# Kernel optimization log

Measured on AMD Instinct MI355X. Metric: run time of the kernel, lower is better.

The kernel has to match this reference:

```python
import jax, jax.numpy as jnp
import numpy as np

NUM_REGIONS = 196
NHEAD = 8
EPS = 1e-8  # torch F.cosine_similarity eps


def _mha(q_in, k_in, v_in, w_in, w_out):
    # q_in,k_in,v_in: (L,B,d); w_in: (3d,d); w_out: (d,d); bias=False, eval (no dropout)
    L, B, d = q_in.shape
    hd = d // NHEAD
    wq, wk, wv = w_in[:d], w_in[d:2 * d], w_in[2 * d:]

    def split_heads(x, w):
        y = x @ w.T  # (L,B,d)
        return jnp.transpose(y.reshape(x.shape[0], B, NHEAD, hd), (1, 2, 0, 3))  # (B,H,L,hd)

    q = split_heads(q_in, wq) * (1.0 / np.sqrt(hd)).astype(q_in.dtype)
    k = split_heads(k_in, wk)
    v = split_heads(v_in, wv)
    attn = jax.nn.softmax(jnp.einsum('bhqd,bhkd->bhqk', q, k), axis=-1)
    out = jnp.einsum('bhqk,bhkd->bhqd', attn, v)  # (B,H,L,hd)
    out = jnp.transpose(out, (2, 0, 1, 3)).reshape(L, B, d)
    return out @ w_out.T


def _window_agg(text, window, anchor):
    # text: (B,T,C); window size W=window (odd); anchor: (B,T,C)
    B, T, C = text.shape
    pad = window // 2
    padded = jnp.pad(text, ((0, 0), (pad, pad), (0, 0)))
    # (B,T,W,C): window k-th element for output pos j is padded[:, j+k]
    win = jnp.stack([padded[:, k:k + T] for k in range(window)], axis=2)
    dot = jnp.einsum('btc,btwc->btw', anchor, win)
    na = jnp.linalg.norm(anchor, axis=-1)          # (B,T)
    nw = jnp.linalg.norm(win, axis=-1)             # (B,T,W)
    weight = dot / (jnp.maximum(na, EPS)[..., None] * jnp.maximum(nw, EPS))
    return jnp.einsum('btw,btwc->btc', weight, win)


def setup_inputs() -> dict:
    key = jax.random.key(0)
    ks = jax.random.split(key, 10)
    L, B, d = 512, 32, 768
    s = 1.0 / np.sqrt(d)
    inp = {
        'query': jax.random.normal(ks[0], (L, B, d), jnp.float32),
        'key': jax.random.normal(ks[1], (L, B, d), jnp.float32),
        'value': jax.random.normal(ks[2], (L, B, d), jnp.float32),
        'w_in1': jax.random.normal(ks[3], (3 * d, d), jnp.float32) * s,
        'w_out1': jax.random.normal(ks[4], (d, d), jnp.float32) * s,
        'w_in2': jax.random.normal(ks[5], (3 * d, d), jnp.float32) * s,
        'w_out2': jax.random.normal(ks[6], (d, d), jnp.float32) * s,
        'w_in3': jax.random.normal(ks[7], (3 * d, d), jnp.float32) * s,
        'w_out3': jax.random.normal(ks[8], (d, d), jnp.float32) * s,
        'alpha': jnp.float32(1.0),
        'beta': jnp.float32(1.0),
        'gamma': jnp.float32(1.0),
    }
    return inp


def reference(query, key, value, w_in1, w_out1, w_in2, w_out2, w_in3, w_out3, alpha, beta, gamma):
    # query/key/value: (L,B,C)
    q_blc = jnp.transpose(query, (1, 0, 2))  # (B,L,C)
    visual = q_blc[:, :NUM_REGIONS]
    text = q_blc[:, NUM_REGIONS:]             # (B,T,C)

    # two-neighbor: anchor is the token itself
    two = _window_agg(text, 3, text)
    # three-neighbor: original code uses padded_two[:, i] with i=j+2, i.e. text shifted
    # left by one with a trailing zero row (faithful to the source's indexing)
    anchor3 = jnp.concatenate([text[:, 1:], jnp.zeros_like(text[:, :1])], axis=1)
    three = _window_agg(text, 5, anchor3)

    two_q = jnp.transpose(jnp.concatenate([visual, two], axis=1), (1, 0, 2))    # (L,B,C)
    three_q = jnp.transpose(jnp.concatenate([visual, three], axis=1), (1, 0, 2))

    out1 = _mha(query, key, value, w_in1, w_out1)
    out2 = _mha(two_q, key, value, w_in2, w_out2)
    out3 = _mha(three_q, key, value, w_in3, w_out3)
    return alpha * out1 + beta * out2 + gamma * out3
```

## Files before the change

### kernel.cpp

```cpp
#include <hip/hip_runtime.h>
#include <cstdint>
#include <cstddef>

typedef __bf16 bf16_t;
typedef float f32x4 __attribute__((ext_vector_type(4)));
typedef __bf16 bf16x8 __attribute__((ext_vector_type(8)));

#define MFMA_BF16(a, b, c) __builtin_amdgcn_mfma_f32_16x16x32_bf16((a), (b), (c), 0, 0, 0)

__global__ void convert_kernel(const float* __restrict__ src,
                               bf16_t* __restrict__ dst, int n8)
{
    const int i = blockIdx.x * blockDim.x + threadIdx.x;
    if (i < n8) {
        const float4* s = (const float4*)src + (size_t)i * 2;
        const float4 a = s[0], b = s[1];
        bf16x8 v = {(bf16_t)a.x, (bf16_t)a.y, (bf16_t)a.z, (bf16_t)a.w,
                    (bf16_t)b.x, (bf16_t)b.y, (bf16_t)b.z, (bf16_t)b.w};
        *((bf16x8*)dst + i) = v;
    }
}

template <typename CT>
__global__ __launch_bounds__(256) void gemm_bt(const bf16_t* __restrict__ A,
                                               const bf16_t* __restrict__ W,
                                               CT* C,
                                               int M, int N, int K,
                                               const float* __restrict__ scale_ptr,
                                               int accumulate)
{
    __shared__ bf16_t As[128 * 32];
    __shared__ bf16_t Ws[128 * 32];
    const int t = threadIdx.x;
    const int lane = t & 63;
    const int w = t >> 6;
    const int wr = (w >> 1) * 64;
    const int wc = (w & 1) * 64;
    const int tm = blockIdx.x * 128, tn = blockIdx.y * 128;
    const int l15 = lane & 15, l4 = lane >> 4;

    const f32x4 fzero = {0.f, 0.f, 0.f, 0.f};
    f32x4 acc[4][4];
    for (int i = 0; i < 4; ++i)
        for (int j = 0; j < 4; ++j) acc[i][j] = fzero;

    const int f0 = t * 8, f1 = f0 + 2048;
    const int ar0 = f0 >> 5, ac0 = f0 & 31;
    const int ar1 = f1 >> 5, ac1 = f1 & 31;

    for (int kb = 0; kb < K; kb += 32) {
        bf16x8 a0 = *(const bf16x8*)(A + (size_t)(tm + ar0) * K + kb + ac0);
        bf16x8 a1 = *(const bf16x8*)(A + (size_t)(tm + ar1) * K + kb + ac1);
        bf16x8 w0 = *(const bf16x8*)(W + (size_t)(tn + ar0) * K + kb + ac0);
        bf16x8 w1 = *(const bf16x8*)(W + (size_t)(tn + ar1) * K + kb + ac1);
        __syncthreads();
        *(bf16x8*)(As + f0) = a0;
        *(bf16x8*)(As + f1) = a1;
        *(bf16x8*)(Ws + f0) = w0;
        *(bf16x8*)(Ws + f1) = w1;
        __syncthreads();
        bf16x8 af[4], bfr[4];
#pragma unroll
        for (int i = 0; i < 4; ++i)
            af[i] = *(const bf16x8*)(As + (wr + i * 16 + l15) * 32 + l4 * 8);
#pragma unroll
        for (int j = 0; j < 4; ++j)
            bfr[j] = *(const bf16x8*)(Ws + (wc + j * 16 + l15) * 32 + l4 * 8);
#pragma unroll
        for (int i = 0; i < 4; ++i)
#pragma unroll
            for (int j = 0; j < 4; ++j)
                acc[i][j] = MFMA_BF16(af[i], bfr[j], acc[i][j]);
    }

    const float scale = scale_ptr ? scale_ptr[0] : 1.0f;
    for (int i = 0; i < 4; ++i) {
        for (int j = 0; j < 4; ++j) {
            const int col = tn + wc + j * 16 + l15;
            for (int r = 0; r < 4; ++r) {
                const int row = tm + wr + i * 16 + l4 * 4 + r;
                const size_t idx = (size_t)row * N + col;
                float v = acc[i][j][r] * scale;
                if (accumulate) v += (float)C[idx];
                C[idx] = (CT)v;
            }
        }
    }
}

__global__ __launch_bounds__(256) void attn_kernel(bf16_t* QC,
                                                   const bf16_t* __restrict__ Kp,
                                                   const bf16_t* __restrict__ Vp)
{
    constexpr int B = 32, HD = 96, D = 768;
    __shared__ bf16_t Ks[64 * 96];
    __shared__ bf16_t Vt[96 * 64];
    __shared__ bf16_t Ps[4 * 16 * 64];

    const int qt = blockIdx.x, h = blockIdx.y, b = blockIdx.z;
    const int t = threadIdx.x, lane = t & 63, w = t >> 6;
    const int l15 = lane & 15, l4 = lane >> 4;
    const int q0 = qt * 64 + w * 16;
    const float qk_scale = 0.10206207261596575f;

    bf16x8 aq[3];
#pragma unroll
    for (int kk = 0; kk < 3; ++kk)
        aq[kk] = *(const bf16x8*)(QC + ((size_t)(q0 + l15) * B + b) * D + h * HD + kk * 32 + l4 * 8);

    const f32x4 fzero = {0.f, 0.f, 0.f, 0.f};
    f32x4 o[6];
#pragma unroll
    for (int f = 0; f < 6; ++f) o[f] = fzero;
    float mr[4], lr[4];
#pragma unroll
    for (int r = 0; r < 4; ++r) { mr[r] = -1e30f; lr[r] = 0.f; }

    for (int kt = 0; kt < 8; ++kt) {
        const int k0 = kt * 64;
        bf16x8 kreg[3], vreg[3];
        int rrs[3], ccs[3];
#pragma unroll
        for (int i = 0; i < 3; ++i) {
            const int f = t * 8 + i * 2048;
            const int rr = f / 96, cc = f % 96;
            rrs[i] = rr; ccs[i] = cc;
            kreg[i] = *(const bf16x8*)(Kp + ((size_t)(k0 + rr) * B + b) * D + h * HD + cc);
            vreg[i] = *(const bf16x8*)(Vp + ((size_t)(k0 + rr) * B + b) * D + h * HD + cc);
        }
        __syncthreads();
#pragma unroll
        for (int i = 0; i < 3; ++i) {
            *(bf16x8*)(Ks + rrs[i] * 96 + ccs[i]) = kreg[i];
#pragma unroll
            for (int j = 0; j < 8; ++j)
                Vt[(ccs[i] + j) * 64 + rrs[i]] = vreg[i][j];
        }
        __syncthreads();

        f32x4 s[4];
#pragma unroll
        for (int n = 0; n < 4; ++n) {
            s[n] = fzero;
#pragma unroll
            for (int kk = 0; kk < 3; ++kk) {
                bf16x8 kf = *(const bf16x8*)(Ks + (n * 16 + l15) * 96 + kk * 32 + l4 * 8);
                s[n] = MFMA_BF16(aq[kk], kf, s[n]);
            }
        }

        float pm[4];
#pragma unroll
        for (int r = 0; r < 4; ++r) {
            float v = fmaxf(fmaxf(s[0][r], s[1][r]), fmaxf(s[2][r], s[3][r]));
            v *= qk_scale;
            v = fmaxf(v, __shfl_xor(v, 1));
            v = fmaxf(v, __shfl_xor(v, 2));
            v = fmaxf(v, __shfl_xor(v, 4));
            v = fmaxf(v, __shfl_xor(v, 8));
            pm[r] = v;
        }
        float corr[4];
        float p[4][4];
#pragma unroll
        for (int r = 0; r < 4; ++r) {
            const float mnew = fmaxf(mr[r], pm[r]);
            corr[r] = __expf(mr[r] - mnew);
            mr[r] = mnew;
            float ps = 0.f;
#pragma unroll
            for (int n = 0; n < 4; ++n) {
                const float pv = __expf(s[n][r] * qk_scale - mnew);
                p[n][r] = pv;
                ps += pv;
            }
            ps += __shfl_xor(ps, 1);
            ps += __shfl_xor(ps, 2);
            ps += __shfl_xor(ps, 4);
            ps += __shfl_xor(ps, 8);
            lr[r] = lr[r] * corr[r] + ps;
        }
#pragma unroll
        for (int f = 0; f < 6; ++f)
#pragma unroll
            for (int r = 0; r < 4; ++r) o[f][r] *= corr[r];

#pragma unroll
        for (int n = 0; n < 4; ++n)
#pragma unroll
            for (int r = 0; r < 4; ++r)
                Ps[w * 1024 + (l4 * 4 + r) * 64 + n * 16 + l15] = (bf16_t)p[n][r];
        asm volatile("s_waitcnt lgkmcnt(0)" ::: "memory");

#pragma unroll
        for (int kk = 0; kk < 2; ++kk) {
            bf16x8 pa = *(const bf16x8*)(Ps + w * 1024 + l15 * 64 + kk * 32 + l4 * 8);
#pragma unroll
            for (int f = 0; f < 6; ++f) {
                bf16x8 vb = *(const bf16x8*)(Vt + (f * 16 + l15) * 64 + kk * 32 + l4 * 8);
                o[f] = MFMA_BF16(pa, vb, o[f]);
            }
        }
    }

#pragma unroll
    for (int f = 0; f < 6; ++f)
#pragma unroll
        for (int r = 0; r < 4; ++r) {
            const int row = q0 + l4 * 4 + r;
            QC[((size_t)row * B + b) * D + h * HD + f * 16 + l15] = (bf16_t)(o[f][r] / lr[r]);
        }
}

__global__ void window_kernel(const float* __restrict__ q,
                              bf16_t* __restrict__ two_q,
                              bf16_t* __restrict__ three_q)
{
    constexpr int T = 316, B = 32, D = 768, NR = 196;
    constexpr float EPS = 1e-8f;
    const int tp = blockIdx.x, b = blockIdx.y, lane = threadIdx.x;

    float val[5][12];
#pragma unroll
    for (int w = 0; w < 5; ++w) {
        const int tt = tp + w - 2;
        const bool ok = (tt >= 0 && tt < T);
#pragma unroll
        for (int j = 0; j < 12; ++j) {
            const int c = lane + 64 * j;
            val[w][j] = ok ? q[((size_t)(NR + tt) * B + b) * D + c] : 0.f;
        }
    }
    float nrm[5], d2[3], d3[5];
#pragma unroll
    for (int w = 0; w < 5; ++w) {
        float s = 0.f;
        for (int j = 0; j < 12; ++j) s += val[w][j] * val[w][j];
        nrm[w] = s;
    }
#pragma unroll
    for (int k = 0; k < 3; ++k) {
        float s = 0.f;
        for (int j = 0; j < 12; ++j) s += val[2][j] * val[k + 1][j];
        d2[k] = s;
    }
#pragma unroll
    for (int k = 0; k < 5; ++k) {
        float s = 0.f;
        for (int j = 0; j < 12; ++j) s += val[3][j] * val[k][j];
        d3[k] = s;
    }
#pragma unroll
    for (int w = 0; w < 5; ++w)
        for (int m = 1; m < 64; m <<= 1) nrm[w] += __shfl_xor(nrm[w], m);
#pragma unroll
    for (int k = 0; k < 3; ++k)
        for (int m = 1; m < 64; m <<= 1) d2[k] += __shfl_xor(d2[k], m);
#pragma unroll
    for (int k = 0; k < 5; ++k)
        for (int m = 1; m < 64; m <<= 1) d3[k] += __shfl_xor(d3[k], m);

    const float na2 = fmaxf(sqrtf(nrm[2]), EPS);
    const float na3 = fmaxf(sqrtf(nrm[3]), EPS);
    float w2[3], w3[5];
#pragma unroll
    for (int k = 0; k < 3; ++k) w2[k] = d2[k] / (na2 * fmaxf(sqrtf(nrm[k + 1]), EPS));
#pragma unroll
    for (int k = 0; k < 5; ++k) w3[k] = d3[k] / (na3 * fmaxf(sqrtf(nrm[k]), EPS));

#pragma unroll
    for (int j = 0; j < 12; ++j) {
        float o2 = 0.f, o3 = 0.f;
#pragma unroll
        for (int k = 0; k < 3; ++k) o2 += w2[k] * val[k + 1][j];
#pragma unroll
        for (int k = 0; k < 5; ++k) o3 += w3[k] * val[k][j];
        const int c = lane + 64 * j;
        const size_t idx = ((size_t)(NR + tp) * B + b) * D + c;
        two_q[idx] = (bf16_t)o2;
        three_q[idx] = (bf16_t)o3;
    }
}

__global__ void copy_visual(const bf16_t* __restrict__ qb,
                            bf16_t* __restrict__ two_q,
                            bf16_t* __restrict__ three_q)
{
    const size_t i = (size_t)blockIdx.x * blockDim.x + threadIdx.x;
    const size_t n = (size_t)196 * 32 * 768 / 8;
    if (i < n) {
        bf16x8 v = *((const bf16x8*)qb + i);
        *((bf16x8*)two_q + i) = v;
        *((bf16x8*)three_q + i) = v;
    }
}

extern "C" void kernel_launch(void* const* d_in, const int* in_sizes, int n_in,
                              void* d_out, int out_size, void* d_ws, size_t ws_size,
                              hipStream_t stream)
{
    const float* query  = (const float*)d_in[0];
    const float* key    = (const float*)d_in[1];
    const float* value  = (const float*)d_in[2];
    const float* w_in[3]  = {(const float*)d_in[3], (const float*)d_in[5], (const float*)d_in[7]};
    const float* w_out[3] = {(const float*)d_in[4], (const float*)d_in[6], (const float*)d_in[8]};
    const float* alpha  = (const float*)d_in[9];
    const float* beta   = (const float*)d_in[10];
    const float* gamma  = (const float*)d_in[11];
    float* out = (float*)d_out;

    const size_t NE = (size_t)512 * 32 * 768;
    const size_t WSZ = (size_t)768 * 768;
    bf16_t* qb      = (bf16_t*)d_ws;
    bf16_t* kb      = qb + NE;
    bf16_t* vb      = kb + NE;
    bf16_t* two_q   = vb + NE;
    bf16_t* three_q = two_q + NE;
    bf16_t* QP      = three_q + NE;
    bf16_t* KP      = QP + NE;
    bf16_t* VP      = KP + NE;
    bf16_t* wb_in[3]  = {VP + NE, VP + NE + 3 * WSZ, VP + NE + 6 * WSZ};
    bf16_t* wb_out[3] = {VP + NE + 9 * WSZ, VP + NE + 10 * WSZ, VP + NE + 11 * WSZ};

    const int cb = 256;
    convert_kernel<<<(int)(NE / 8 + cb - 1) / cb, cb, 0, stream>>>(query, qb, (int)(NE / 8));
    convert_kernel<<<(int)(NE / 8 + cb - 1) / cb, cb, 0, stream>>>(key, kb, (int)(NE / 8));
    convert_kernel<<<(int)(NE / 8 + cb - 1) / cb, cb, 0, stream>>>(value, vb, (int)(NE / 8));
    for (int i = 0; i < 3; ++i) {
        convert_kernel<<<(int)(3 * WSZ / 8 + cb - 1) / cb, cb, 0, stream>>>(w_in[i], wb_in[i], (int)(3 * WSZ / 8));
        convert_kernel<<<(int)(WSZ / 8 + cb - 1) / cb, cb, 0, stream>>>(w_out[i], wb_out[i], (int)(WSZ / 8));
    }

    const int M = 512 * 32, D = 768;
    const dim3 ggrid(M / 128, D / 128);

    copy_visual<<<2352, 256, 0, stream>>>(qb, two_q, three_q);
    window_kernel<<<dim3(316, 32), 64, 0, stream>>>(query, two_q, three_q);

    const bf16_t* qins[3] = {two_q, three_q, qb};
    const int     wsel[3] = {1, 2, 0};
    for (int i = 0; i < 3; ++i) {
        const int s = wsel[i];
        gemm_bt<bf16_t><<<ggrid, 256, 0, stream>>>(qins[i], wb_in[s], QP, M, D, D, nullptr, 0);
        gemm_bt<bf16_t><<<ggrid, 256, 0, stream>>>(kb, wb_in[s] + WSZ, KP, M, D, D, nullptr, 0);
        gemm_bt<bf16_t><<<ggrid, 256, 0, stream>>>(vb, wb_in[s] + 2 * WSZ, VP, M, D, D, nullptr, 0);
        attn_kernel<<<dim3(8, 8, 32), 256, 0, stream>>>(QP, KP, VP);
        const float* sc = (s == 0) ? alpha : (s == 1) ? beta : gamma;
        gemm_bt<float><<<ggrid, 256, 0, stream>>>(QP, wb_out[s], out, M, D, D, sc, i > 0 ? 1 : 0);
    }
}
```

Baseline: 1.106 ms.

## Restructure attention to process full sequence per block; use direct global-to-LDS loads in GEMM

The attention kernel now gives each block one (head, batch) pair with 8 waves, and each wave handles 64 query rows as four 16-row tiles. Each K/V tile is loaded into shared memory once for all 512 queries instead of once per 64-query block, and each K/V fragment read from LDS feeds two query tiles. The V-transpose and P buffers get XOR swizzling to reduce LDS bank conflicts. The GEMM and the attention K-tile load switch to global_load_lds so data goes straight to LDS without passing through registers. In exchange, the grid shrinks from 2048 to 256 blocks and per-thread register use rises, which may limit occupancy and latency hiding.

```diff
diff --git a/kernel.cpp b/kernel.cpp
--- a/kernel.cpp
+++ b/kernel.cpp
@@ -7,6 +7,10 @@
 typedef __bf16 bf16x8 __attribute__((ext_vector_type(8)));
 
 #define MFMA_BF16(a, b, c) __builtin_amdgcn_mfma_f32_16x16x32_bf16((a), (b), (c), 0, 0, 0)
+
+#define GLDS16(gp, lp) __builtin_amdgcn_global_load_lds(                      \
+    (const __attribute__((address_space(1))) void*)(gp),                      \
+    (__attribute__((address_space(3))) void*)(lp), 16, 0, 0)
 
 __global__ void convert_kernel(const float* __restrict__ src,
                                bf16_t* __restrict__ dst, int n8)
@@ -41,23 +45,20 @@
 
     const f32x4 fzero = {0.f, 0.f, 0.f, 0.f};
     f32x4 acc[4][4];
+#pragma unroll
     for (int i = 0; i < 4; ++i)
+#pragma unroll
         for (int j = 0; j < 4; ++j) acc[i][j] = fzero;
 
-    const int f0 = t * 8, f1 = f0 + 2048;
-    const int ar0 = f0 >> 5, ac0 = f0 & 31;
-    const int ar1 = f1 >> 5, ac1 = f1 & 31;
+    const int ar0 = t >> 2, ac0 = (t & 3) * 8;
+    const int ar1 = ar0 + 64;
 
     for (int kb = 0; kb < K; kb += 32) {
-        bf16x8 a0 = *(const bf16x8*)(A + (size_t)(tm + ar0) * K + kb + ac0);
-        bf16x8 a1 = *(const bf16x8*)(A + (size_t)(tm + ar1) * K + kb + ac1);
-        bf16x8 w0 = *(const bf16x8*)(W + (size_t)(tn + ar0) * K + kb + ac0);
-        bf16x8 w1 = *(const bf16x8*)(W + (size_t)(tn + ar1) * K + kb + ac1);
         __syncthreads();
-        *(bf16x8*)(As + f0) = a0;
-        *(bf16x8*)(As + f1) = a1;
-        *(bf16x8*)(Ws + f0) = w0;
-        *(bf16x8*)(Ws + f1) = w1;
+        GLDS16(A + (size_t)(tm + ar0) * K + kb + ac0, (char*)As + w * 1024);
+        GLDS16(A + (size_t)(tm + ar1) * K + kb + ac0, (char*)As + 4096 + w * 1024);
+        GLDS16(W + (size_t)(tn + ar0) * K + kb + ac0, (char*)Ws + w * 1024);
+        GLDS16(W + (size_t)(tn + ar1) * K + kb + ac0, (char*)Ws + 4096 + w * 1024);
         __syncthreads();
         bf16x8 af[4], bfr[4];
 #pragma unroll
@@ -74,9 +75,12 @@
     }
 
     const float scale = scale_ptr ? scale_ptr[0] : 1.0f;
+#pragma unroll
     for (int i = 0; i < 4; ++i) {
+#pragma unroll
         for (int j = 0; j < 4; ++j) {
             const int col = tn + wc + j * 16 + l15;
+#pragma unroll
             for (int r = 0; r < 4; ++r) {
                 const int row = tm + wr + i * 16 + l4 * 4 + r;
                 const size_t idx = (size_t)row * N + col;
@@ -88,128 +92,151 @@
     }
 }
 
-__global__ __launch_bounds__(256) void attn_kernel(bf16_t* QC,
-                                                   const bf16_t* __restrict__ Kp,
-                                                   const bf16_t* __restrict__ Vp)
+__global__ __launch_bounds__(512, 2) void attn_kernel(bf16_t* QC,
+                                                      const bf16_t* __restrict__ Kp,
+                                                      const bf16_t* __restrict__ Vp)
 {
     constexpr int B = 32, HD = 96, D = 768;
     __shared__ bf16_t Ks[64 * 96];
     __shared__ bf16_t Vt[96 * 64];
-    __shared__ bf16_t Ps[4 * 16 * 64];
-
-    const int qt = blockIdx.x, h = blockIdx.y, b = blockIdx.z;
+    __shared__ bf16_t Ps[8][2][16 * 64];
+
+    const int h = blockIdx.x, b = blockIdx.y;
     const int t = threadIdx.x, lane = t & 63, w = t >> 6;
     const int l15 = lane & 15, l4 = lane >> 4;
-    const int q0 = qt * 64 + w * 16;
     const float qk_scale = 0.10206207261596575f;
 
-    bf16x8 aq[3];
-#pragma unroll
-    for (int kk = 0; kk < 3; ++kk)
-        aq[kk] = *(const bf16x8*)(QC + ((size_t)(q0 + l15) * B + b) * D + h * HD + kk * 32 + l4 * 8);
+    bf16x8 aq[4][3];
+#pragma unroll
+    for (int m = 0; m < 4; ++m)
+#pragma unroll
+        for (int kk = 0; kk < 3; ++kk)
+            aq[m][kk] = *(const bf16x8*)(QC + ((size_t)(w * 64 + m * 16 + l15) * B + b) * D
+                                         + h * HD + kk * 32 + l4 * 8);
 
     const f32x4 fzero = {0.f, 0.f, 0.f, 0.f};
-    f32x4 o[6];
-#pragma unroll
-    for (int f = 0; f < 6; ++f) o[f] = fzero;
-    float mr[4], lr[4];
-#pragma unroll
-    for (int r = 0; r < 4; ++r) { mr[r] = -1e30f; lr[r] = 0.f; }
+    f32x4 o[4][6];
+#pragma unroll
+    for (int m = 0; m < 4; ++m)
+#pragma unroll
+        for (int f = 0; f < 6; ++f) o[m][f] = fzero;
+    float mr[4][4], lr[4][4];
+#pragma unroll
+    for (int m = 0; m < 4; ++m)
+#pragma unroll
+        for (int r = 0; r < 4; ++r) { mr[m][r] = -1e30f; lr[m][r] = 0.f; }
+
+    const int f0 = t * 8;
+    const int rr0 = f0 / 96, cc0 = f0 % 96;
+    const int f1 = 4096 + t * 8;
+    const int rr1 = f1 / 96, cc1 = f1 % 96;
+    const int sv0 = ((cc0 >> 3) & 7) << 3;
+    const int sv1 = ((cc1 >> 3) & 7) << 3;
 
     for (int kt = 0; kt < 8; ++kt) {
         const int k0 = kt * 64;
-        bf16x8 kreg[3], vreg[3];
-        int rrs[3], ccs[3];
-#pragma unroll
-        for (int i = 0; i < 3; ++i) {
-            const int f = t * 8 + i * 2048;
-            const int rr = f / 96, cc = f % 96;
-            rrs[i] = rr; ccs[i] = cc;
-            kreg[i] = *(const bf16x8*)(Kp + ((size_t)(k0 + rr) * B + b) * D + h * HD + cc);
-            vreg[i] = *(const bf16x8*)(Vp + ((size_t)(k0 + rr) * B + b) * D + h * HD + cc);
-        }
         __syncthreads();
-#pragma unroll
-        for (int i = 0; i < 3; ++i) {
-            *(bf16x8*)(Ks + rrs[i] * 96 + ccs[i]) = kreg[i];
+        GLDS16(Kp + ((size_t)(k0 + rr0) * B + b) * D + h * HD + cc0,
+               (char*)Ks + w * 1024);
+        if (w < 4)
+            GLDS16(Kp + ((size_t)(k0 + rr1) * B + b) * D + h * HD + cc1,
+                   (char*)Ks + 8192 + w * 1024);
+        bf16x8 v0 = *(const bf16x8*)(Vp + ((size_t)(k0 + rr0) * B + b) * D + h * HD + cc0);
+        {
+            const int colsw = rr0 ^ sv0;
 #pragma unroll
             for (int j = 0; j < 8; ++j)
-                Vt[(ccs[i] + j) * 64 + rrs[i]] = vreg[i][j];
+                Vt[(cc0 + j) * 64 + colsw] = v0[j];
+        }
+        if (w < 4) {
+            bf16x8 v1 = *(const bf16x8*)(Vp + ((size_t)(k0 + rr1) * B + b) * D + h * HD + cc1);
+            const int colsw = rr1 ^ sv1;
+#pragma unroll
+            for (int j = 0; j < 8; ++j)
+                Vt[(cc1 + j) * 64 + colsw] = v1[j];
         }
         __syncthreads();
 
-        f32x4 s[4];
-#pragma unroll
-        for (int n = 0; n < 4; ++n) {
-            s[n] = fzero;
-#pragma unroll
-            for (int kk = 0; kk < 3; ++kk) {
-                bf16x8 kf = *(const bf16x8*)(Ks + (n * 16 + l15) * 96 + kk * 32 + l4 * 8);
-                s[n] = MFMA_BF16(aq[kk], kf, s[n]);
+#pragma unroll
+        for (int mp = 0; mp < 2; ++mp) {
+            f32x4 s[2][4];
+#pragma unroll
+            for (int mi = 0; mi < 2; ++mi)
+#pragma unroll
+                for (int n = 0; n < 4; ++n) s[mi][n] = fzero;
+#pragma unroll
+            for (int kk = 0; kk < 3; ++kk)
+#pragma unroll
+                for (int n = 0; n < 4; ++n) {
+                    bf16x8 kf = *(const bf16x8*)(Ks + (n * 16 + l15) * 96 + kk * 32 + l4 * 8);
+                    s[0][n] = MFMA_BF16(aq[2 * mp][kk], kf, s[0][n]);
+                    s[1][n] = MFMA_BF16(aq[2 * mp + 1][kk], kf, s[1][n]);
+                }
+#pragma unroll
+            for (int mi = 0; mi < 2; ++mi) {
+                const int m = 2 * mp + mi;
+#pragma unroll
+                for (int r = 0; r < 4; ++r) {
+                    float v = fmaxf(fmaxf(s[mi][0][r], s[mi][1][r]),
+                                    fmaxf(s[mi][2][r], s[mi][3][r]));
+                    v *= qk_scale;
+                    v = fmaxf(v, __shfl_xor(v, 1));
+                    v = fmaxf(v, __shfl_xor(v, 2));
+                    v = fmaxf(v, __shfl_xor(v, 4));
+                    v = fmaxf(v, __shfl_xor(v, 8));
+                    const float mnew = fmaxf(mr[m][r], v);
+                    const float corr = __expf(mr[m][r] - mnew);
+                    mr[m][r] = mnew;
+                    const int row = 4 * l4 + r;
+                    float ps = 0.f;
+#pragma unroll
+                    for (int n = 0; n < 4; ++n) {
+                        const float pv = __expf(s[mi][n][r] * qk_scale - mnew);
+                        ps += pv;
+                        Ps[w][mi][row * 64 + ((n * 16 + l15) ^ ((row & 7) << 3))] = (bf16_t)pv;
+                    }
+                    ps += __shfl_xor(ps, 1);
+                    ps += __shfl_xor(ps, 2);
+                    ps += __shfl_xor(ps, 4);
+                    ps += __shfl_xor(ps, 8);
+                    lr[m][r] = lr[m][r] * corr + ps;
+#pragma unroll
+                    for (int f = 0; f < 6; ++f) o[m][f][r] *= corr;
+                }
             }
-        }
-
-        float pm[4];
-#pragma unroll
-        for (int r = 0; r < 4; ++r) {
-            float v = fmaxf(fmaxf(s[0][r], s[1][r]), fmaxf(s[2][r], s[3][r]));
-            v *= qk_scale;
-            v = fmaxf(v, __shfl_xor(v, 1));
-            v = fmaxf(v, __shfl_xor(v, 2));
-            v = fmaxf(v, __shfl_xor(v, 4));
-            v = fmaxf(v, __shfl_xor(v, 8));
-            pm[r] = v;
-        }
-        float corr[4];
-        float p[4][4];
-#pragma unroll
-        for (int r = 0; r < 4; ++r) {
-            const float mnew = fmaxf(mr[r], pm[r]);
-            corr[r] = __expf(mr[r] - mnew);
-            mr[r] = mnew;
-            float ps = 0.f;
-#pragma unroll
-            for (int n = 0; n < 4; ++n) {
-                const float pv = __expf(s[n][r] * qk_scale - mnew);
-                p[n][r] = pv;
-                ps += pv;
+            asm volatile("s_waitcnt lgkmcnt(0)" ::: "memory");
+            __builtin_amdgcn_sched_barrier(0);
+            bf16x8 pa[2][2];
+#pragma unroll
+            for (int mi = 0; mi < 2; ++mi)
+#pragma unroll
+                for (int kk = 0; kk < 2; ++kk)
+                    pa[mi][kk] = *(const bf16x8*)(&Ps[w][mi][l15 * 64 +
+                                  ((kk * 32 + l4 * 8) ^ ((l15 & 7) << 3))]);
+#pragma unroll
+            for (int f = 0; f < 6; ++f) {
+                const int c = f * 16 + l15;
+                const int sv = ((c >> 3) & 7) << 3;
+#pragma unroll
+                for (int kk = 0; kk < 2; ++kk) {
+                    bf16x8 vbf = *(const bf16x8*)(Vt + c * 64 + ((kk * 32 + l4 * 8) ^ sv));
+                    o[2 * mp][f]     = MFMA_BF16(pa[0][kk], vbf, o[2 * mp][f]);
+                    o[2 * mp + 1][f] = MFMA_BF16(pa[1][kk], vbf, o[2 * mp + 1][f]);
+                }
             }
-            ps += __shfl_xor(ps, 1);
-            ps += __shfl_xor(ps, 2);
-            ps += __shfl_xor(ps, 4);
-            ps += __shfl_xor(ps, 8);
-            lr[r] = lr[r] * corr[r] + ps;
-        }
+        }
+    }
+
+#pragma unroll
+    for (int m = 0; m < 4; ++m)
 #pragma unroll
         for (int f = 0; f < 6; ++f)
 #pragma unroll
-            for (int r = 0; r < 4; ++r) o[f][r] *= corr[r];
-
-#pragma unroll
-        for (int n = 0; n < 4; ++n)
-#pragma unroll
-            for (int r = 0; r < 4; ++r)
-                Ps[w * 1024 + (l4 * 4 + r) * 64 + n * 16 + l15] = (bf16_t)p[n][r];
-        asm volatile("s_waitcnt lgkmcnt(0)" ::: "memory");
-
-#pragma unroll
-        for (int kk = 0; kk < 2; ++kk) {
-            bf16x8 pa = *(const bf16x8*)(Ps + w * 1024 + l15 * 64 + kk * 32 + l4 * 8);
-#pragma unroll
-            for (int f = 0; f < 6; ++f) {
-                bf16x8 vb = *(const bf16x8*)(Vt + (f * 16 + l15) * 64 + kk * 32 + l4 * 8);
-                o[f] = MFMA_BF16(pa, vb, o[f]);
+            for (int r = 0; r < 4; ++r) {
+                const int row = w * 64 + m * 16 + 4 * l4 + r;
+                QC[((size_t)row * B + b) * D + h * HD + f * 16 + l15] =
+                    (bf16_t)(o[m][f][r] / lr[m][r]);
             }
-        }
-    }
-
-#pragma unroll
-    for (int f = 0; f < 6; ++f)
-#pragma unroll
-        for (int r = 0; r < 4; ++r) {
-            const int row = q0 + l4 * 4 + r;
-            QC[((size_t)row * B + b) * D + h * HD + f * 16 + l15] = (bf16_t)(o[f][r] / lr[r]);
-        }
 }
 
 __global__ void window_kernel(const float* __restrict__ q,
@@ -344,7 +371,7 @@
         gemm_bt<bf16_t><<<ggrid, 256, 0, stream>>>(qins[i], wb_in[s], QP, M, D, D, nullptr, 0);
         gemm_bt<bf16_t><<<ggrid, 256, 0, stream>>>(kb, wb_in[s] + WSZ, KP, M, D, D, nullptr, 0);
         gemm_bt<bf16_t><<<ggrid, 256, 0, stream>>>(vb, wb_in[s] + 2 * WSZ, VP, M, D, D, nullptr, 0);
-        attn_kernel<<<dim3(8, 8, 32), 256, 0, stream>>>(QP, KP, VP);
+        attn_kernel<<<dim3(8, 32), 512, 0, stream>>>(QP, KP, VP);
         const float* sc = (s == 0) ? alpha : (s == 1) ? beta : gamma;
         gemm_bt<float><<<ggrid, 256, 0, stream>>>(QP, wb_out[s], out, M, D, D, sc, i > 0 ? 1 : 0);
     }
```

After: 977.4 us. 11.6% less time.
